# Kernel tuning notes

Measured on AMD Instinct MI355X. Metric: run time of the kernel, lower is better.

The kernel has to match this reference:

```python
import jax, jax.numpy as jnp
from jax import lax
import numpy as np

NUM_TOKENS = 14
DIM = 512
B, T = 32, 512


def _lstm(xs, W_ih, W_hh, b_ih, b_hh):
    """PyTorch-semantics single-layer LSTM, batch_first. xs: [B,T,D] -> hs: [B,T,D].
    Gate order i, f, g, o; gates = x @ W_ih^T + b_ih + h @ W_hh^T + b_hh."""
    Bsz, Tlen, D = xs.shape
    # Precompute input contribution for all timesteps (one big GEMM).
    pre = jnp.einsum('btd,gd->btg', xs, W_ih) + (b_ih + b_hh)  # [B,T,4D]

    def step(carry, p):
        h, c = carry
        gates = p + h @ W_hh.T  # [B,4D]
        i, f, g, o = jnp.split(gates, 4, axis=-1)
        i = jax.nn.sigmoid(i)
        f = jax.nn.sigmoid(f)
        g = jnp.tanh(g)
        o = jax.nn.sigmoid(o)
        c = f * c + i * g
        h = o * jnp.tanh(c)
        return (h, c), h

    h0 = jnp.zeros((Bsz, D), xs.dtype)
    (_, _), hs = lax.scan(step, (h0, h0), jnp.swapaxes(pre, 0, 1))  # time-major scan
    return jnp.swapaxes(hs, 0, 1)  # [B,T,D]


def setup_inputs() -> dict:
    key = jax.random.key(0)
    ks = jax.random.split(key, 10)
    s_emb = 1.0  # nn.Embedding default init N(0,1)
    s = 1.0 / np.sqrt(DIM)  # nn.LSTM default init U(-1/sqrt(H), 1/sqrt(H))
    u = lambda k, shape: jax.random.uniform(k, shape, jnp.float32, -s, s)
    return {
        'x': jax.random.randint(ks[0], (B, T), 0, NUM_TOKENS, dtype=jnp.int32),
        'embed': jax.random.normal(ks[1], (NUM_TOKENS, DIM), jnp.float32) * s_emb,
        'W_ih_q': u(ks[2], (4 * DIM, DIM)),
        'W_hh_q': u(ks[3], (4 * DIM, DIM)),
        'b_ih_q': u(ks[4], (4 * DIM,)),
        'b_hh_q': u(ks[5], (4 * DIM,)),
        'W_ih_k': u(ks[6], (4 * DIM, DIM)),
        'W_hh_k': u(ks[7], (4 * DIM, DIM)),
        'b_ih_k': u(ks[8], (4 * DIM,)),
        'b_hh_k': u(ks[9], (4 * DIM,)),
    }


def reference(x, embed, W_ih_q, W_hh_q, b_ih_q, b_hh_q, W_ih_k, W_hh_k, b_ih_k, b_hh_k):
    e = embed[x]  # [B,T,D] embedding lookup
    q = _lstm(e, W_ih_q, W_hh_q, b_ih_q, b_hh_q)  # [B,T,D]
    k = _lstm(e, W_ih_k, W_hh_k, b_ih_k, b_hh_k)  # [B,T,D]
    A = jnp.einsum('btd,bsd->bts', q, k)  # bmm(q, k^T) -> [B,T,T]
    return A
```

## Files before the change

### kernel.cpp

```cpp
#include <hip/hip_runtime.h>
#include <hip/hip_bf16.h>


#define TB 32
#define TT 512
#define TD 512
#define NTOK 14

typedef __attribute__((ext_vector_type(8))) short short8;
typedef __attribute__((ext_vector_type(4))) float f32x4;
typedef __attribute__((ext_vector_type(4))) unsigned int u32x4;

__device__ __forceinline__ float fsigmoid(float v) { return 1.f / (1.f + __expf(-v)); }
__device__ __forceinline__ float ftanh(float v) {
    float a = fabsf(v);
    float e = __expf(-2.f * a);
    float r = (1.f - e) / (1.f + e);
    return copysignf(r, v);
}
__device__ __forceinline__ unsigned int f2bf(float f) {
    __hip_bfloat16 h = __float2bfloat16(f);
    return (unsigned int)__builtin_bit_cast(unsigned short, h);
}

__device__ __forceinline__ u32x4 load16_coh(const unsigned int* p) {
    u32x4 r;
    asm volatile("global_load_dwordx4 %0, %1, off sc0 sc1" : "=v"(r) : "v"(p));
    return r;
}
__device__ __forceinline__ void store4_coh(unsigned int* p, unsigned int v) {
    asm volatile("global_store_dword %0, %1, off sc0 sc1" :: "v"(p), "v"(v) : "memory");
}

__global__ __launch_bounds__(256) void pre_tab_kernel(
    const float* __restrict__ embed,
    const float* __restrict__ Wih_q, const float* __restrict__ bih_q, const float* __restrict__ bhh_q,
    const float* __restrict__ Wih_k, const float* __restrict__ bih_k, const float* __restrict__ bhh_k,
    float* __restrict__ pre)
{
    int idx = blockIdx.x * 256 + threadIdx.x;
    int l = idx / (NTOK * 4 * TD);
    int r = idx % (NTOK * 4 * TD);
    int tok = r / (4 * TD), j = r % (4 * TD);
    const float* Wih = l ? Wih_k : Wih_q;
    float acc = l ? (bih_k[j] + bhh_k[j]) : (bih_q[j] + bhh_q[j]);
    const float4* e4 = (const float4*)(embed + (size_t)tok * TD);
    const float4* w4 = (const float4*)(Wih + (size_t)j * TD);
    for (int t2 = 0; t2 < TD / 4; ++t2) {
        float4 e = e4[t2], w = w4[t2];
        acc += e.x * w.x + e.y * w.y + e.z * w.z + e.w * w.w;
    }
    pre[idx] = acc;
}

__global__ __launch_bounds__(256) void init_hbf(unsigned int* hbf) {
    hbf[blockIdx.x * 256 + threadIdx.x] = 0;
}

__global__ __launch_bounds__(256) void lstm_persist(
    const float* __restrict__ Whh_q, const float* __restrict__ Whh_k,
    const float* __restrict__ pre,
    const int* __restrict__ x,
    float* __restrict__ qout, float* __restrict__ kout,
    unsigned int* __restrict__ hbf)
{
    __shared__ unsigned short w_lds[64][512];
    __shared__ unsigned short h_lds[16][512];
    __shared__ float          g_lds[64][17];
    __shared__ unsigned char  x_lds[16 * TT];
    __shared__ float          pre_lds[NTOK][64];

    int wg  = blockIdx.x;
    int l   = wg >> 6;
    int g   = (wg >> 5) & 1;
    int wid = wg & 31;
    int d0  = wid << 4;
    int tid = threadIdx.x;
    int lane = tid & 63;
    int rt  = tid >> 6;

    const float* Whh = l ? Whh_k : Whh_q;
    float* hist = l ? kout : qout;
    unsigned int* hb_l = hbf + (size_t)l * 2 * TB * TD;

    {
        int r = tid >> 2;
        const float* src = Whh + (size_t)((r >> 4) * TD + d0 + (r & 15)) * TD;
#pragma unroll
        for (int i = 0; i < 16; ++i) {
            int c = (tid & 3) + 4 * i;
            float4 a = ((const float4*)src)[c * 2];
            float4 b4 = ((const float4*)src)[c * 2 + 1];
            unsigned short* dst = &w_lds[r][(c ^ (r & 7)) * 8];
            dst[0] = (unsigned short)f2bf(a.x); dst[1] = (unsigned short)f2bf(a.y);
            dst[2] = (unsigned short)f2bf(a.z); dst[3] = (unsigned short)f2bf(a.w);
            dst[4] = (unsigned short)f2bf(b4.x); dst[5] = (unsigned short)f2bf(b4.y);
            dst[6] = (unsigned short)f2bf(b4.z); dst[7] = (unsigned short)f2bf(b4.w);
        }
    }
    for (int i = tid; i < 16 * TT; i += 256)
        x_lds[i] = (unsigned char)x[(g * 16 + (i >> 9)) * TT + (i & 511)];
    for (int i = tid; i < NTOK * 64; i += 256) {
        int tok = i >> 6, j = i & 63;
        pre_lds[tok][j] = pre[((size_t)l * NTOK + tok) * (4 * TD) + (j >> 4) * TD + d0 + (j & 15)];
    }
    __syncthreads();

    int bl = tid >> 4, dd = tid & 15;
    int bg = g * 16 + bl;
    float creg = 0.f;

    {
        int tok = x_lds[bl * TT];
        float i_ = fsigmoid(pre_lds[tok][dd]);
        float f_ = fsigmoid(pre_lds[tok][16 + dd]);
        float g_ = ftanh(pre_lds[tok][32 + dd]);
        float o_ = fsigmoid(pre_lds[tok][48 + dd]);
        creg = i_ * g_;
        float h = o_ * ftanh(creg);
        store4_coh(hb_l + (size_t)bg * TD + d0 + dd, (f2bf(h) << 16) | 1u);
        hist[((size_t)bg * TT) * TD + d0 + dd] = h;
    }

    for (int t = 1; t < TT; ++t) {
        {
            const unsigned int e = (unsigned int)t;
            int row = tid >> 4;
            const unsigned int* hb = hb_l + (size_t)((t - 1) & 1) * TB * TD
                                          + (size_t)(g * 16 + row) * TD;
            u32x4 A0[4], B0[4];
#pragma unroll
            for (int j = 0; j < 4; ++j) {
                int m = (tid & 15) + 16 * j;
                A0[j] = load16_coh(hb + m * 8);
                B0[j] = load16_coh(hb + m * 8 + 4);
            }
            unsigned int st = 0xFu;
            for (;;) {
                asm volatile("s_waitcnt vmcnt(0)" ::: "memory");
                __builtin_amdgcn_sched_barrier(0);
                unsigned int ns = 0;
#pragma unroll
                for (int j = 0; j < 4; ++j) if (st & (1u << j)) {
                    unsigned int bad =
                        ((A0[j].x ^ e) | (A0[j].y ^ e) | (A0[j].z ^ e) | (A0[j].w ^ e) |
                         (B0[j].x ^ e) | (B0[j].y ^ e) | (B0[j].z ^ e) | (B0[j].w ^ e)) & 0xffffu;
                    if (bad) ns |= 1u << j;
                }
                st = ns;
                if (!__any(st != 0)) break;
#pragma unroll
                for (int j = 0; j < 4; ++j) if (st & (1u << j)) {
                    int m = (tid & 15) + 16 * j;
                    A0[j] = load16_coh(hb + m * 8);
                    B0[j] = load16_coh(hb + m * 8 + 4);
                }
                __builtin_amdgcn_s_sleep(1);
            }
#pragma unroll
            for (int j = 0; j < 4; ++j) {
                int m = (tid & 15) + 16 * j;
                u32x4 o;
                o.x = (A0[j].x >> 16) | (A0[j].y & 0xffff0000u);
                o.y = (A0[j].z >> 16) | (A0[j].w & 0xffff0000u);
                o.z = (B0[j].x >> 16) | (B0[j].y & 0xffff0000u);
                o.w = (B0[j].z >> 16) | (B0[j].w & 0xffff0000u);
                *(u32x4*)&h_lds[row][(m ^ (row & 7)) * 8] = o;
            }
        }
        __syncthreads();

        {
            f32x4 acc = {0.f, 0.f, 0.f, 0.f};
            int rr = rt * 16 + (lane & 15);
            int hr = lane & 15;
#pragma unroll
            for (int kk = 0; kk < 16; ++kk) {
                int c = kk * 4 + (lane >> 4);
                short8 a  = *(const short8*)&h_lds[hr][(c ^ (hr & 7)) * 8];
                short8 bf = *(const short8*)&w_lds[rr][(c ^ (rr & 7)) * 8];
                acc = __builtin_amdgcn_mfma_f32_16x16x32_bf16(a, bf, acc, 0, 0, 0);
            }
            int gb = (lane >> 4) << 2;
#pragma unroll
            for (int r2 = 0; r2 < 4; ++r2) g_lds[rr][gb + r2] = acc[r2];
        }
        __syncthreads();

        {
            int tok = x_lds[bl * TT + t];
            float gi = g_lds[dd][bl]      + pre_lds[tok][dd];
            float gf = g_lds[16 + dd][bl] + pre_lds[tok][16 + dd];
            float gg = g_lds[32 + dd][bl] + pre_lds[tok][32 + dd];
            float go = g_lds[48 + dd][bl] + pre_lds[tok][48 + dd];
            float i_ = fsigmoid(gi), f_ = fsigmoid(gf), g2 = ftanh(gg), o_ = fsigmoid(go);
            creg = f_ * creg + i_ * g2;
            float h = o_ * ftanh(creg);
            store4_coh(hb_l + (size_t)(t & 1) * TB * TD + (size_t)bg * TD + d0 + dd,
                       (f2bf(h) << 16) | (unsigned int)(t + 1));
            hist[((size_t)bg * TT + t) * TD + d0 + dd] = h;
        }
    }
}

__global__ __launch_bounds__(256) void qk_gemm(
    const float* __restrict__ q, const float* __restrict__ k, float* __restrict__ A)
{
    __shared__ float qs[64][68];
    __shared__ float ks[64][68];
    int b = blockIdx.y;
    int t0 = (blockIdx.x >> 3) * 64;
    int s0 = (blockIdx.x & 7) * 64;
    const float* qb = q + (size_t)b * TT * TD;
    const float* kb = k + (size_t)b * TT * TD;
    int tid = threadIdx.x;
    int ty = tid >> 4, tx = tid & 15;
    float accr[4][4] = {};
    for (int k0 = 0; k0 < TD; k0 += 64) {
        for (int i = tid; i < 64 * 16; i += 256) {
            int r = i >> 4, c4 = i & 15;
            ((float4*)&qs[r][0])[c4] = ((const float4*)(qb + (size_t)(t0 + r) * TD + k0))[c4];
            ((float4*)&ks[r][0])[c4] = ((const float4*)(kb + (size_t)(s0 + r) * TD + k0))[c4];
        }
        __syncthreads();
#pragma unroll 4
        for (int kk = 0; kk < 64; kk += 4) {
            float4 qv[4], kv[4];
#pragma unroll
            for (int i = 0; i < 4; ++i) qv[i] = *(const float4*)&qs[ty * 4 + i][kk];
#pragma unroll
            for (int j = 0; j < 4; ++j) kv[j] = *(const float4*)&ks[tx * 4 + j][kk];
#pragma unroll
            for (int i = 0; i < 4; ++i)
#pragma unroll
                for (int j = 0; j < 4; ++j)
                    accr[i][j] += qv[i].x * kv[j].x + qv[i].y * kv[j].y
                                + qv[i].z * kv[j].z + qv[i].w * kv[j].w;
        }
        __syncthreads();
    }
    for (int i = 0; i < 4; ++i)
        for (int j = 0; j < 4; ++j)
            A[(size_t)b * TT * TT + (size_t)(t0 + ty * 4 + i) * TT + (s0 + tx * 4 + j)] = accr[i][j];
}

extern "C" void kernel_launch(void* const* d_in, const int* in_sizes, int n_in,
                              void* d_out, int out_size, void* d_ws, size_t ws_size,
                              hipStream_t stream)
{
    const int*   x      = (const int*)d_in[0];
    const float* embed  = (const float*)d_in[1];
    const float* Wih_q  = (const float*)d_in[2];
    const float* Whh_q  = (const float*)d_in[3];
    const float* bih_q  = (const float*)d_in[4];
    const float* bhh_q  = (const float*)d_in[5];
    const float* Wih_k  = (const float*)d_in[6];
    const float* Whh_k  = (const float*)d_in[7];
    const float* bih_k  = (const float*)d_in[8];
    const float* bhh_k  = (const float*)d_in[9];

    float* ws   = (float*)d_ws;
    float* q    = ws;
    float* kbuf = q + (size_t)TB * TT * TD;
    float* pre  = kbuf + (size_t)TB * TT * TD;
    unsigned int* hbf = (unsigned int*)(pre + 2 * NTOK * 4 * TD);

    init_hbf<<<256, 256, 0, stream>>>(hbf);
    pre_tab_kernel<<<224, 256, 0, stream>>>(embed, Wih_q, bih_q, bhh_q,
                                            Wih_k, bih_k, bhh_k, pre);
    lstm_persist<<<128, 256, 0, stream>>>(Whh_q, Whh_k, pre, x, q, kbuf, hbf);
    dim3 g2(64, 32);
    qk_gemm<<<g2, 256, 0, stream>>>(q, kbuf, (float*)d_out);
}
```

Baseline: 1.701 ms.

## Replace per-element tagged h exchange with per-workgroup flag synchronization

The hidden-state exchange between persistent workgroups used to pack a bf16 value with a step tag into every 32-bit word, and each consumer polled all the words it needed. Now h is stored as plain bf16 shorts, and each workgroup waits for its stores to drain, runs a barrier, and publishes a single step flag. Consumers poll 32 flags before doing one bulk load of h. This halves exchange traffic and shrinks the polling set, but it adds a store drain, an extra __syncthreads per step and a flag round trip on the critical path.

Result: faster. 1.651 ms (-2.9%).

```diff
diff --git a/kernel.cpp b/kernel.cpp
--- a/kernel.cpp
+++ b/kernel.cpp
@@ -9,7 +9,6 @@
 
 typedef __attribute__((ext_vector_type(8))) short short8;
 typedef __attribute__((ext_vector_type(4))) float f32x4;
-typedef __attribute__((ext_vector_type(4))) unsigned int u32x4;
 
 __device__ __forceinline__ float fsigmoid(float v) { return 1.f / (1.f + __expf(-v)); }
 __device__ __forceinline__ float ftanh(float v) {
@@ -23,13 +22,22 @@
     return (unsigned int)__builtin_bit_cast(unsigned short, h);
 }
 
-__device__ __forceinline__ u32x4 load16_coh(const unsigned int* p) {
-    u32x4 r;
+__device__ __forceinline__ short8 load16_coh(const unsigned short* p) {
+    short8 r;
     asm volatile("global_load_dwordx4 %0, %1, off sc0 sc1" : "=v"(r) : "v"(p));
     return r;
 }
+__device__ __forceinline__ void store2_coh(unsigned short* p, unsigned int v) {
+    asm volatile("global_store_short %0, %1, off sc0 sc1" :: "v"(p), "v"(v) : "memory");
+}
 __device__ __forceinline__ void store4_coh(unsigned int* p, unsigned int v) {
     asm volatile("global_store_dword %0, %1, off sc0 sc1" :: "v"(p), "v"(v) : "memory");
+}
+__device__ __forceinline__ unsigned int load4_coh(const unsigned int* p) {
+    unsigned int r;
+    asm volatile("global_load_dword %0, %1, off sc0 sc1\n\ts_waitcnt vmcnt(0)"
+                 : "=v"(r) : "v"(p) : "memory");
+    return r;
 }
 
 __global__ __launch_bounds__(256) void pre_tab_kernel(
@@ -53,16 +61,15 @@
     pre[idx] = acc;
 }
 
-__global__ __launch_bounds__(256) void init_hbf(unsigned int* hbf) {
-    hbf[blockIdx.x * 256 + threadIdx.x] = 0;
-}
+__global__ void init_flags(unsigned int* flags) { flags[threadIdx.x] = 0; }
 
 __global__ __launch_bounds__(256) void lstm_persist(
     const float* __restrict__ Whh_q, const float* __restrict__ Whh_k,
     const float* __restrict__ pre,
     const int* __restrict__ x,
     float* __restrict__ qout, float* __restrict__ kout,
-    unsigned int* __restrict__ hbf)
+    unsigned short* __restrict__ hbf,
+    unsigned int* __restrict__ flags)
 {
     __shared__ unsigned short w_lds[64][512];
     __shared__ unsigned short h_lds[16][512];
@@ -81,7 +88,8 @@
 
     const float* Whh = l ? Whh_k : Whh_q;
     float* hist = l ? kout : qout;
-    unsigned int* hb_l = hbf + (size_t)l * 2 * TB * TD;
+    unsigned short* hb_l = hbf + (size_t)l * 2 * TB * TD;
+    unsigned int* fl = flags + (l * 2 + g) * 32;
 
     {
         int r = tid >> 2;
@@ -118,55 +126,36 @@
         float o_ = fsigmoid(pre_lds[tok][48 + dd]);
         creg = i_ * g_;
         float h = o_ * ftanh(creg);
-        store4_coh(hb_l + (size_t)bg * TD + d0 + dd, (f2bf(h) << 16) | 1u);
+        store2_coh(hb_l + (size_t)bg * TD + d0 + dd, f2bf(h));
         hist[((size_t)bg * TT) * TD + d0 + dd] = h;
-    }
+        asm volatile("s_waitcnt vmcnt(0)" ::: "memory");
+    }
+    __syncthreads();
+    if (tid == 0) store4_coh(fl + wid, 1u);
 
     for (int t = 1; t < TT; ++t) {
         {
-            const unsigned int e = (unsigned int)t;
-            int row = tid >> 4;
-            const unsigned int* hb = hb_l + (size_t)((t - 1) & 1) * TB * TD
-                                          + (size_t)(g * 16 + row) * TD;
-            u32x4 A0[4], B0[4];
-#pragma unroll
-            for (int j = 0; j < 4; ++j) {
-                int m = (tid & 15) + 16 * j;
-                A0[j] = load16_coh(hb + m * 8);
-                B0[j] = load16_coh(hb + m * 8 + 4);
-            }
-            unsigned int st = 0xFu;
+            unsigned int need = (unsigned int)t;
             for (;;) {
-                asm volatile("s_waitcnt vmcnt(0)" ::: "memory");
-                __builtin_amdgcn_sched_barrier(0);
-                unsigned int ns = 0;
-#pragma unroll
-                for (int j = 0; j < 4; ++j) if (st & (1u << j)) {
-                    unsigned int bad =
-                        ((A0[j].x ^ e) | (A0[j].y ^ e) | (A0[j].z ^ e) | (A0[j].w ^ e) |
-                         (B0[j].x ^ e) | (B0[j].y ^ e) | (B0[j].z ^ e) | (B0[j].w ^ e)) & 0xffffu;
-                    if (bad) ns |= 1u << j;
-                }
-                st = ns;
-                if (!__any(st != 0)) break;
-#pragma unroll
-                for (int j = 0; j < 4; ++j) if (st & (1u << j)) {
-                    int m = (tid & 15) + 16 * j;
-                    A0[j] = load16_coh(hb + m * 8);
-                    B0[j] = load16_coh(hb + m * 8 + 4);
-                }
+                unsigned int v = load4_coh(fl + (lane & 31));
+                if (__all((int)(v >= need))) break;
                 __builtin_amdgcn_s_sleep(1);
             }
-#pragma unroll
-            for (int j = 0; j < 4; ++j) {
-                int m = (tid & 15) + 16 * j;
-                u32x4 o;
-                o.x = (A0[j].x >> 16) | (A0[j].y & 0xffff0000u);
-                o.y = (A0[j].z >> 16) | (A0[j].w & 0xffff0000u);
-                o.z = (B0[j].x >> 16) | (B0[j].y & 0xffff0000u);
-                o.w = (B0[j].z >> 16) | (B0[j].w & 0xffff0000u);
-                *(u32x4*)&h_lds[row][(m ^ (row & 7)) * 8] = o;
-            }
+        }
+        {
+            int row = tid >> 4;
+            const unsigned short* hb = hb_l + (size_t)((t - 1) & 1) * TB * TD
+                                            + (size_t)(g * 16 + row) * TD;
+            short8 v0 = load16_coh(hb + ((tid & 15) +  0) * 8);
+            short8 v1 = load16_coh(hb + ((tid & 15) + 16) * 8);
+            short8 v2 = load16_coh(hb + ((tid & 15) + 32) * 8);
+            short8 v3 = load16_coh(hb + ((tid & 15) + 48) * 8);
+            asm volatile("s_waitcnt vmcnt(0)" ::: "memory");
+            __builtin_amdgcn_sched_barrier(0);
+            *(short8*)&h_lds[row][(((tid & 15) +  0) ^ (row & 7)) * 8] = v0;
+            *(short8*)&h_lds[row][(((tid & 15) + 16) ^ (row & 7)) * 8] = v1;
+            *(short8*)&h_lds[row][(((tid & 15) + 32) ^ (row & 7)) * 8] = v2;
+            *(short8*)&h_lds[row][(((tid & 15) + 48) ^ (row & 7)) * 8] = v3;
         }
         __syncthreads();
 
@@ -196,10 +185,12 @@
             float i_ = fsigmoid(gi), f_ = fsigmoid(gf), g2 = ftanh(gg), o_ = fsigmoid(go);
             creg = f_ * creg + i_ * g2;
             float h = o_ * ftanh(creg);
-            store4_coh(hb_l + (size_t)(t & 1) * TB * TD + (size_t)bg * TD + d0 + dd,
-                       (f2bf(h) << 16) | (unsigned int)(t + 1));
+            store2_coh(hb_l + (size_t)(t & 1) * TB * TD + (size_t)bg * TD + d0 + dd, f2bf(h));
             hist[((size_t)bg * TT + t) * TD + d0 + dd] = h;
-        }
+            asm volatile("s_waitcnt vmcnt(0)" ::: "memory");
+        }
+        __syncthreads();
+        if (tid == 0) store4_coh(fl + wid, (unsigned int)(t + 1));
     }
 }
 
@@ -263,12 +254,13 @@
     float* q    = ws;
     float* kbuf = q + (size_t)TB * TT * TD;
     float* pre  = kbuf + (size_t)TB * TT * TD;
-    unsigned int* hbf = (unsigned int*)(pre + 2 * NTOK * 4 * TD);
-
-    init_hbf<<<256, 256, 0, stream>>>(hbf);
+    unsigned short* hbf = (unsigned short*)(pre + 2 * NTOK * 4 * TD);
+    unsigned int* flags = (unsigned int*)(hbf + 65536);
+
+    init_flags<<<1, 128, 0, stream>>>(flags);
     pre_tab_kernel<<<224, 256, 0, stream>>>(embed, Wih_q, bih_q, bhh_q,
                                             Wih_k, bih_k, bhh_k, pre);
-    lstm_persist<<<128, 256, 0, stream>>>(Whh_q, Whh_k, pre, x, q, kbuf, hbf);
+    lstm_persist<<<128, 256, 0, stream>>>(Whh_q, Whh_k, pre, x, q, kbuf, hbf, flags);
     dim3 g2(64, 32);
     qk_gemm<<<g2, 256, 0, stream>>>(q, kbuf, (float*)d_out);
 }
```
